# Kernel tuning notes

Hardware: AMD Instinct MI355X
Metric: run time of the kernel (lower is better)

## Reference

```python
import jax, jax.numpy as jnp
import numpy as np

NUM_NODES = 100000
EMBED_DIM = 64
NUM_LAYERS = 3
NUM_EDGES = 3200000


def setup_inputs() -> dict:
    key = jax.random.key(0)
    k_emb, k_edge = jax.random.split(key)
    # Learned node embedding table (PyG LightGCN initializes with xavier-like; values don't matter for correctness)
    emb = jax.random.normal(k_emb, (NUM_NODES, EMBED_DIM), dtype=jnp.float32) * 0.1
    edge_index = jax.random.randint(k_edge, (2, NUM_EDGES), 0, NUM_NODES, dtype=jnp.int64)
    return {"emb": emb, "edge_index": edge_index}


def _lightgcn_embedding(emb, edge_index):
    """Faithful to PyG LightGCN.get_embedding with LGConv (gcn_norm, add_self_loops=False)."""
    n = emb.shape[0]
    src, dst = edge_index[0], edge_index[1]
    # symmetric normalization: deg computed by scatter of ones onto col (dst)
    deg = jax.ops.segment_sum(jnp.ones(src.shape[0], dtype=emb.dtype), dst, num_segments=n)
    deg_inv_sqrt = jnp.where(deg > 0, jax.lax.rsqrt(jnp.maximum(deg, 1.0)), 0.0)
    w = deg_inv_sqrt[src] * deg_inv_sqrt[dst]  # [E]

    x = emb
    out = emb  # alpha-weighted sum; uniform alpha = 1/(num_layers+1)
    for _ in range(NUM_LAYERS):
        # SpMM: out[dst] += w * x[src]
        x = jax.ops.segment_sum(w[:, None] * x[src], dst, num_segments=n)
        out = out + x
    return out / (NUM_LAYERS + 1)


def reference(emb, edge_index):
    return _lightgcn_embedding(emb, edge_index)
```

## Files before the change

### kernel.cpp

```cpp
#include <hip/hip_runtime.h>
#include <hip/hip_bf16.h>

typedef __hip_bfloat16 bf16;
typedef float          f32x4 __attribute__((ext_vector_type(4)));
typedef unsigned short u16x4 __attribute__((ext_vector_type(4)));

#define N_NODES  100000
#define EMBED    64
#define N_EDGES  3200000
#define ND       6400000
#define N_LAYERS 3

#define PNB  256
#define BSZ  391
#define EPB  4096
#define NSL  8
#define SLW  12512
#define R8   (BSZ * NSL)

#define NSPL 4


__global__ void k_flags0(int* f, int* bcnt) {
    int t = threadIdx.x;
    if (t < 16) f[t] = 0;
    bcnt[t] = 0;
}

__global__ void __launch_bounds__(256) k_scan(const uint4* __restrict__ edge4,
                                              const uint4* __restrict__ emb4,
                                              int* __restrict__ fl) {
    __shared__ int red[256];
    __shared__ int rodd[256];
    int t = threadIdx.x;
    int gid = blockIdx.x * 256 + t;
    int step = gridDim.x * 256;

    unsigned odd = 0;
    const int NV_E = (2 * N_EDGES) / 4;
    int i = gid;
    for (; i + 3 * step < NV_E; i += 4 * step) {
        uint4 v0 = edge4[i];
        uint4 v1 = edge4[i + step];
        uint4 v2 = edge4[i + 2 * step];
        uint4 v3 = edge4[i + 3 * step];
        odd |= v0.y | v0.w | v1.y | v1.w | v2.y | v2.w | v3.y | v3.w;
    }
    for (; i < NV_E; i += step) {
        uint4 v = edge4[i];
        odd |= v.y | v.w;
    }

    int local = 0;
    const int NV_M = ND / 8;
#define CEN8(v)                                                          \
    {                                                                    \
        unsigned b;                                                      \
        b = ((v).x >> 8)  & 0x7f; if (b < 0x2e || b > 0x41) local++;     \
        b = ((v).x >> 24) & 0x7f; if (b < 0x2e || b > 0x41) local++;     \
        b = ((v).y >> 8)  & 0x7f; if (b < 0x2e || b > 0x41) local++;     \
        b = ((v).y >> 24) & 0x7f; if (b < 0x2e || b > 0x41) local++;     \
        b = ((v).z >> 8)  & 0x7f; if (b < 0x2e || b > 0x41) local++;     \
        b = ((v).z >> 24) & 0x7f; if (b < 0x2e || b > 0x41) local++;     \
        b = ((v).w >> 8)  & 0x7f; if (b < 0x2e || b > 0x41) local++;     \
        b = ((v).w >> 24) & 0x7f; if (b < 0x2e || b > 0x41) local++;     \
    }
    i = gid;
    for (; i + 3 * step < NV_M; i += 4 * step) {
        uint4 v0 = emb4[i];
        uint4 v1 = emb4[i + step];
        uint4 v2 = emb4[i + 2 * step];
        uint4 v3 = emb4[i + 3 * step];
        CEN8(v0); CEN8(v1); CEN8(v2); CEN8(v3);
    }
    for (; i < NV_M; i += step) {
        uint4 v = emb4[i];
        CEN8(v);
    }
#undef CEN8

    red[t] = local;
    rodd[t] = (odd != 0);
    __syncthreads();
    for (int s2 = 128; s2 > 0; s2 >>= 1) {
        if (t < s2) { red[t] += red[t + s2]; rodd[t] |= rodd[t + s2]; }
        __syncthreads();
    }
    if (t == 0) {
        if (red[0]) atomicAdd(&fl[1], red[0]);
        if (rodd[0]) atomicOr(&fl[0], 1);
    }
}

__device__ __forceinline__ int is_i64(const int* fl) { return fl[0] == 0; }
__device__ __forceinline__ int rd_src(const int* e, int i64, int k) {
    return i64 ? e[2 * k] : e[k];
}
__device__ __forceinline__ int rd_dst(const int* e, int i64, int k) {
    return i64 ? e[2 * (N_EDGES + k)] : e[N_EDGES + k];
}
__device__ __forceinline__ int clampid(int v) {
    return (v < 0) ? 0 : ((v >= N_NODES) ? (N_NODES - 1) : v);
}
__device__ __forceinline__ float rd_emb(const void* emb, const int* fl, int i) {
    if (fl[1] < (ND / 16)) return __bfloat162float(((const bf16*)emb)[i]);
    return ((const float*)emb)[i];
}

__global__ void __launch_bounds__(256) k_bcnt(const int* __restrict__ edge,
                                              const int* __restrict__ fl,
                                              int* __restrict__ bcnt) {
    __shared__ int h[PNB];
    int t = threadIdx.x;
    h[t] = 0;
    __syncthreads();
    const uint4* e4 = (const uint4*)edge;
    int gid = blockIdx.x * 256 + t;
    int step = gridDim.x * 256;
    if (is_i64(fl)) {
        const int base = N_EDGES / 2;
        const int nv   = N_EDGES / 2;
        for (int i = gid; i < nv; i += step) {
            uint4 v = e4[base + i];
            atomicAdd(&h[clampid((int)v.x) / BSZ], 1);
            atomicAdd(&h[clampid((int)v.z) / BSZ], 1);
        }
    } else {
        const int base = N_EDGES / 4;
        const int nv   = N_EDGES / 4;
        for (int i = gid; i < nv; i += step) {
            uint4 v = e4[base + i];
            atomicAdd(&h[clampid((int)v.x) / BSZ], 1);
            atomicAdd(&h[clampid((int)v.y) / BSZ], 1);
            atomicAdd(&h[clampid((int)v.z) / BSZ], 1);
            atomicAdd(&h[clampid((int)v.w) / BSZ], 1);
        }
    }
    __syncthreads();
    if (h[t]) atomicAdd(&bcnt[t], h[t]);
}

__global__ void __launch_bounds__(256) k_bscan(const int* __restrict__ bcnt,
                                               int* __restrict__ bbase,
                                               int* __restrict__ bcur) {
    __shared__ int sb[PNB];
    int t = threadIdx.x;
    int c = bcnt[t];
    sb[t] = c;
    __syncthreads();
    for (int off = 1; off < PNB; off <<= 1) {
        int v = (t >= off) ? sb[t - off] : 0;
        __syncthreads();
        sb[t] += v;
        __syncthreads();
    }
    int ex = sb[t] - c;
    bbase[t] = ex;
    bcur[t] = ex;
    if (t == PNB - 1) bbase[PNB] = sb[t];
}

__global__ void __launch_bounds__(256) k_part(const int* __restrict__ edge,
                                              const int* __restrict__ fl,
                                              int* __restrict__ bcur,
                                              uint2* __restrict__ pairs) {
    __shared__ int h[PNB];
    __shared__ int excl[PNB];
    __shared__ int gbase[PNB];
    __shared__ int lcur[PNB];
    __shared__ uint2 st[EPB];
    __shared__ unsigned char binof[EPB];
    int t = threadIdx.x;
    int e0 = blockIdx.x * EPB;
    int nval = N_EDGES - e0;
    if (nval > EPB) nval = EPB;
    int i64 = is_i64(fl);

    h[t] = 0;
    __syncthreads();
    for (int k = t; k < nval; k += 256) {
        int d = clampid(rd_dst(edge, i64, e0 + k));
        atomicAdd(&h[d / BSZ], 1);
    }
    __syncthreads();
    int c = h[t];
    excl[t] = c;
    __syncthreads();
    for (int off = 1; off < 256; off <<= 1) {
        int v = (t >= off) ? excl[t - off] : 0;
        __syncthreads();
        excl[t] += v;
        __syncthreads();
    }
    int myexcl = excl[t] - c;
    __syncthreads();
    excl[t] = myexcl;
    gbase[t] = (c > 0) ? atomicAdd(&bcur[t], c) : 0;
    lcur[t] = myexcl;
    __syncthreads();
    for (int k = t; k < nval; k += 256) {
        int s = clampid(rd_src(edge, i64, e0 + k));
        int d = clampid(rd_dst(edge, i64, e0 + k));
        int b = d / BSZ;
        int lp = atomicAdd(&lcur[b], 1);
        st[lp] = make_uint2((unsigned)s, (unsigned)d);
        binof[lp] = (unsigned char)b;
    }
    __syncthreads();
    for (int k = t; k < nval; k += 256) {
        int b = binof[k];
        pairs[gbase[b] + (k - excl[b])] = st[k];
    }
}

__global__ void __launch_bounds__(1024) k_build(const uint2* __restrict__ pairs,
                                                const int* __restrict__ bbase,
                                                int* __restrict__ rp2,
                                                float* __restrict__ dis,
                                                int* __restrict__ csr) {
    __shared__ int hh[R8];
    __shared__ int rt[512];
    int b = blockIdx.x;
    int t = threadIdx.x;
    int base = b * BSZ;
    for (int i = t; i < R8; i += 1024) hh[i] = 0;
    __syncthreads();
    int beg = bbase[b], end = bbase[b + 1];
    for (int i = beg + t; i < end; i += 1024) {
        uint2 p = pairs[i];
        int r = (int)p.y - base;
        int s = (int)p.x / SLW;
        atomicAdd(&hh[r * NSL + s], 1);
    }
    __syncthreads();
    int rtot = 0;
    if (t < BSZ) {
        int o = 0;
        for (int k = 0; k < NSL; k++) {
            int cc = hh[t * NSL + k];
            hh[t * NSL + k] = o;
            o += cc;
        }
        rtot = o;
    }
    if (t < 512) rt[t] = (t < BSZ) ? rtot : 0;
    __syncthreads();
    for (int off = 1; off < 512; off <<= 1) {
        int v = 0;
        if (t < 512 && t >= off) v = rt[t - off];
        __syncthreads();
        if (t < 512 && t >= off) rt[t] += v;
        __syncthreads();
    }
    if (t < BSZ) {
        int gb = beg + (rt[t] - rtot);
        int n = base + t;
        if (n < N_NODES) {
            dis[n] = (rtot > 0) ? rsqrtf((float)rtot) : 0.0f;
            for (int k = 0; k < NSL; k++) rp2[n * NSL + k] = gb + hh[t * NSL + k];
            if (n == N_NODES - 1) rp2[N_NODES * NSL] = N_EDGES;
        }
        for (int k = 0; k < NSL; k++) hh[t * NSL + k] += gb;
    }
    __syncthreads();
    for (int i = beg + t; i < end; i += 1024) {
        uint2 p = pairs[i];
        int r = (int)p.y - base;
        int s = (int)p.x / SLW;
        int pos = atomicAdd(&hh[r * NSL + s], 1);
        csr[pos] = (int)p.x;
    }
}

__global__ void k_init(const void* __restrict__ emb, const int* __restrict__ fl,
                       const float* __restrict__ dis,
                       float* __restrict__ out, bf16* __restrict__ Y) {
    int i = blockIdx.x * blockDim.x + threadIdx.x;
    if (i < ND) {
        float v = rd_emb(emb, fl, i);
        out[i] = v;
        int n = i >> 6, cc = i & 63;
        Y[(size_t)(cc >> 4) * (N_NODES * 16) + n * 16 + (cc & 15)] =
            __float2bfloat16(dis[n] * v);
    }
}

#define GATHER4(SRC)                                                     \
    {                                                                    \
        uint2 v = *(const uint2*)(Ys + (SRC) * 8 + c * 2);               \
        a0 += __uint_as_float(v.x << 16);                                \
        a1 += __uint_as_float(v.x & 0xffff0000u);                        \
        a2 += __uint_as_float(v.y << 16);                                \
        a3 += __uint_as_float(v.y & 0xffff0000u);                        \
    }

__global__ void __launch_bounds__(256) k_spmm(
        const int* __restrict__ rp2, const int* __restrict__ csr,
        const float* __restrict__ dis, const bf16* __restrict__ Yin,
        float* __restrict__ out, bf16* __restrict__ Yout, int last) {
    int bid = blockIdx.x;
    int xcd = bid & 7;
    int s = xcd >> 1;
    int rowblk = (bid >> 3) * 2 + (xcd & 1);
    int wave = threadIdx.x >> 6;
    int lane = threadIdx.x & 63;
    int g = lane >> 4;
    int l = lane & 15;
    int e = l >> 2;
    int c = l & 3;
    int n = rowblk * 16 + wave * 4 + g;
    if (n >= N_NODES) return;
    int beg = rp2[n * NSL];
    int end = rp2[(n + 1) * NSL];
    const unsigned* Ys = (const unsigned*)Yin + (size_t)s * (N_NODES * 8);
    float a0 = 0.f, a1 = 0.f, a2 = 0.f, a3 = 0.f;
    int j = beg;
    for (; j + 16 <= end; j += 16) {
        int s0 = csr[j + e];
        int s1 = csr[j + 4 + e];
        int s2 = csr[j + 8 + e];
        int s3 = csr[j + 12 + e];
        GATHER4(s0);
        GATHER4(s1);
        GATHER4(s2);
        GATHER4(s3);
    }
    for (; j + 8 <= end; j += 8) {
        int s0 = csr[j + e];
        int s1 = csr[j + 4 + e];
        GATHER4(s0);
        GATHER4(s1);
    }
    if (j + e < end)     { int sv = csr[j + e];     GATHER4(sv); }
    if (j + 4 + e < end) { int sv = csr[j + 4 + e]; GATHER4(sv); }
    a0 += __shfl_xor(a0, 4); a0 += __shfl_xor(a0, 8);
    a1 += __shfl_xor(a1, 4); a1 += __shfl_xor(a1, 8);
    a2 += __shfl_xor(a2, 4); a2 += __shfl_xor(a2, 8);
    a3 += __shfl_xor(a3, 4); a3 += __shfl_xor(a3, 8);
    if (e == 0) {
        float dn = dis[n];
        float x0 = dn * a0, x1 = dn * a1, x2 = dn * a2, x3 = dn * a3;
        int i4 = n * 16 + s * 4 + c;
        f32x4 o = __builtin_nontemporal_load((const f32x4*)out + i4);
        if (last) {
            o.x = (o.x + x0) * 0.25f;
            o.y = (o.y + x1) * 0.25f;
            o.z = (o.z + x2) * 0.25f;
            o.w = (o.w + x3) * 0.25f;
            __builtin_nontemporal_store(o, (f32x4*)out + i4);
        } else {
            o.x += x0; o.y += x1; o.z += x2; o.w += x3;
            __builtin_nontemporal_store(o, (f32x4*)out + i4);
            bf16 t0 = __float2bfloat16(dn * x0);
            bf16 t1 = __float2bfloat16(dn * x1);
            bf16 t2 = __float2bfloat16(dn * x2);
            bf16 t3 = __float2bfloat16(dn * x3);
            u16x4 yv;
            yv.x = *(unsigned short*)&t0;
            yv.y = *(unsigned short*)&t1;
            yv.z = *(unsigned short*)&t2;
            yv.w = *(unsigned short*)&t3;
            __builtin_nontemporal_store(
                yv, (u16x4*)Yout + (size_t)s * (N_NODES * 4) + n * 4 + c);
        }
    }
}

__global__ void k_fill42(float* __restrict__ o) {
    int i = blockIdx.x * blockDim.x + threadIdx.x;
    if (i < ND) o[i] = 42.0f;
}

extern "C" void kernel_launch(void* const* d_in, const int* in_sizes, int n_in,
                              void* d_out, int out_size, void* d_ws, size_t ws_size,
                              hipStream_t stream) {
    const void* emb = d_in[0];
    const int* edge = (const int*)d_in[1];
    float* out = (float*)d_out;

    const int B = 256;
    const int gND = (ND + B - 1) / B;
    const int gP  = (N_EDGES + EPB - 1) / EPB;
    const int gS  = 25000;

    char* ws = (char*)d_ws;
    int* fl = (int*)ws;
    size_t off = 256;
    const size_t off_dis   = off;  off += (size_t)N_NODES * 4;
    const size_t off_rp2   = off;  off += (size_t)(N_NODES * NSL + 8) * 4;
    const size_t off_bcnt  = off;  off += 1024;
    const size_t off_bbase = off;  off += 1056;
    const size_t off_bcur  = off;  off += 1024;
    const size_t off_csr   = off;  off += (size_t)N_EDGES * 4;
    const size_t off_Y0    = off;  off += (size_t)ND * 2;
    const size_t off_Y1    = off;  off += (size_t)ND * 2;
    const size_t need = off;

    if (ws_size < need) {
        k_fill42<<<gND, B, 0, stream>>>(out);
        return;
    }

    float* dis   = (float*)(ws + off_dis);
    int*   rp2   = (int*)(ws + off_rp2);
    int*   bcnt  = (int*)(ws + off_bcnt);
    int*   bbase = (int*)(ws + off_bbase);
    int*   bcur  = (int*)(ws + off_bcur);
    int*   csr   = (int*)(ws + off_csr);
    uint2* pairs = (uint2*)(ws + off_Y0);
    bf16*  Y0    = (bf16*)(ws + off_Y0);
    bf16*  Y1    = (bf16*)(ws + off_Y1);

    k_flags0<<<1, 256, 0, stream>>>(fl, bcnt);
    k_scan<<<512, B, 0, stream>>>((const uint4*)edge, (const uint4*)emb, fl);

    k_bcnt<<<1024, B, 0, stream>>>(edge, fl, bcnt);
    k_bscan<<<1, 256, 0, stream>>>(bcnt, bbase, bcur);
    k_part<<<gP, B, 0, stream>>>(edge, fl, bcur, pairs);
    k_build<<<PNB, 1024, 0, stream>>>(pairs, bbase, rp2, dis, csr);

    k_init<<<gND, B, 0, stream>>>(emb, fl, dis, out, Y0);

    k_spmm<<<gS, B, 0, stream>>>(rp2, csr, dis, Y0, out, Y1, 0);
    k_spmm<<<gS, B, 0, stream>>>(rp2, csr, dis, Y1, out, Y0, 0);
    k_spmm<<<gS, B, 0, stream>>>(rp2, csr, dis, Y0, out, Y1, 1);
}
```

Baseline: 504.3 us.

## Detect index width from input size, fuse scan with bin count, widen gathers

The edge-index width is now inferred on the host from the input byte size, which removes the full pass over the edge array that checked for nonzero high words. The dtype check on the embeddings is fused with the destination-bin histogram into a single kernel. The partition kernel reads int64 edges as 16-byte vectors. k_init now writes 8 elements per thread, and the SpMM gathers 16-byte bf16 rows with 8 edges per node group instead of 4. The trade-offs are a dependence on in_sizes for choosing the dtype, more registers per SpMM thread and an extra shuffle stage.

```diff
diff --git a/kernel.cpp b/kernel.cpp
--- a/kernel.cpp
+++ b/kernel.cpp
@@ -27,29 +27,27 @@
     bcnt[t] = 0;
 }
 
-__global__ void __launch_bounds__(256) k_scan(const uint4* __restrict__ edge4,
-                                              const uint4* __restrict__ emb4,
-                                              int* __restrict__ fl) {
+__device__ __forceinline__ int rd_src(const int* e, int i64, int k) {
+    return i64 ? e[2 * k] : e[k];
+}
+__device__ __forceinline__ int rd_dst(const int* e, int i64, int k) {
+    return i64 ? e[2 * (N_EDGES + k)] : e[N_EDGES + k];
+}
+__device__ __forceinline__ int clampid(int v) {
+    return (v < 0) ? 0 : ((v >= N_NODES) ? (N_NODES - 1) : v);
+}
+
+__global__ void __launch_bounds__(256) k_scanb(const int* __restrict__ edge,
+                                               const uint4* __restrict__ emb4,
+                                               int i64, int* __restrict__ fl,
+                                               int* __restrict__ bcnt) {
+    __shared__ int h[PNB];
     __shared__ int red[256];
-    __shared__ int rodd[256];
     int t = threadIdx.x;
     int gid = blockIdx.x * 256 + t;
     int step = gridDim.x * 256;
-
-    unsigned odd = 0;
-    const int NV_E = (2 * N_EDGES) / 4;
-    int i = gid;
-    for (; i + 3 * step < NV_E; i += 4 * step) {
-        uint4 v0 = edge4[i];
-        uint4 v1 = edge4[i + step];
-        uint4 v2 = edge4[i + 2 * step];
-        uint4 v3 = edge4[i + 3 * step];
-        odd |= v0.y | v0.w | v1.y | v1.w | v2.y | v2.w | v3.y | v3.w;
-    }
-    for (; i < NV_E; i += step) {
-        uint4 v = edge4[i];
-        odd |= v.y | v.w;
-    }
+    h[t] = 0;
+    __syncthreads();
 
     int local = 0;
     const int NV_M = ND / 8;
@@ -65,7 +63,7 @@
         b = ((v).w >> 8)  & 0x7f; if (b < 0x2e || b > 0x41) local++;     \
         b = ((v).w >> 24) & 0x7f; if (b < 0x2e || b > 0x41) local++;     \
     }
-    i = gid;
+    int i = gid;
     for (; i + 3 * step < NV_M; i += 4 * step) {
         uint4 v0 = emb4[i];
         uint4 v1 = emb4[i + step];
@@ -79,64 +77,34 @@
     }
 #undef CEN8
 
-    red[t] = local;
-    rodd[t] = (odd != 0);
-    __syncthreads();
-    for (int s2 = 128; s2 > 0; s2 >>= 1) {
-        if (t < s2) { red[t] += red[t + s2]; rodd[t] |= rodd[t + s2]; }
-        __syncthreads();
-    }
-    if (t == 0) {
-        if (red[0]) atomicAdd(&fl[1], red[0]);
-        if (rodd[0]) atomicOr(&fl[0], 1);
-    }
-}
-
-__device__ __forceinline__ int is_i64(const int* fl) { return fl[0] == 0; }
-__device__ __forceinline__ int rd_src(const int* e, int i64, int k) {
-    return i64 ? e[2 * k] : e[k];
-}
-__device__ __forceinline__ int rd_dst(const int* e, int i64, int k) {
-    return i64 ? e[2 * (N_EDGES + k)] : e[N_EDGES + k];
-}
-__device__ __forceinline__ int clampid(int v) {
-    return (v < 0) ? 0 : ((v >= N_NODES) ? (N_NODES - 1) : v);
-}
-__device__ __forceinline__ float rd_emb(const void* emb, const int* fl, int i) {
-    if (fl[1] < (ND / 16)) return __bfloat162float(((const bf16*)emb)[i]);
-    return ((const float*)emb)[i];
-}
-
-__global__ void __launch_bounds__(256) k_bcnt(const int* __restrict__ edge,
-                                              const int* __restrict__ fl,
-                                              int* __restrict__ bcnt) {
-    __shared__ int h[PNB];
-    int t = threadIdx.x;
-    h[t] = 0;
-    __syncthreads();
     const uint4* e4 = (const uint4*)edge;
-    int gid = blockIdx.x * 256 + t;
-    int step = gridDim.x * 256;
-    if (is_i64(fl)) {
+    if (i64) {
         const int base = N_EDGES / 2;
         const int nv   = N_EDGES / 2;
-        for (int i = gid; i < nv; i += step) {
-            uint4 v = e4[base + i];
+        for (int k = gid; k < nv; k += step) {
+            uint4 v = e4[base + k];
             atomicAdd(&h[clampid((int)v.x) / BSZ], 1);
             atomicAdd(&h[clampid((int)v.z) / BSZ], 1);
         }
     } else {
         const int base = N_EDGES / 4;
         const int nv   = N_EDGES / 4;
-        for (int i = gid; i < nv; i += step) {
-            uint4 v = e4[base + i];
+        for (int k = gid; k < nv; k += step) {
+            uint4 v = e4[base + k];
             atomicAdd(&h[clampid((int)v.x) / BSZ], 1);
             atomicAdd(&h[clampid((int)v.y) / BSZ], 1);
             atomicAdd(&h[clampid((int)v.z) / BSZ], 1);
             atomicAdd(&h[clampid((int)v.w) / BSZ], 1);
         }
     }
-    __syncthreads();
+
+    red[t] = local;
+    __syncthreads();
+    for (int s2 = 128; s2 > 0; s2 >>= 1) {
+        if (t < s2) red[t] += red[t + s2];
+        __syncthreads();
+    }
+    if (t == 0 && red[0]) atomicAdd(&fl[1], red[0]);
     if (h[t]) atomicAdd(&bcnt[t], h[t]);
 }
 
@@ -161,7 +129,7 @@
 }
 
 __global__ void __launch_bounds__(256) k_part(const int* __restrict__ edge,
-                                              const int* __restrict__ fl,
+                                              int i64,
                                               int* __restrict__ bcur,
                                               uint2* __restrict__ pairs) {
     __shared__ int h[PNB];
@@ -174,13 +142,22 @@
     int e0 = blockIdx.x * EPB;
     int nval = N_EDGES - e0;
     if (nval > EPB) nval = EPB;
-    int i64 = is_i64(fl);
+    const uint4* e4 = (const uint4*)edge;
 
     h[t] = 0;
     __syncthreads();
-    for (int k = t; k < nval; k += 256) {
-        int d = clampid(rd_dst(edge, i64, e0 + k));
-        atomicAdd(&h[d / BSZ], 1);
+    if (i64) {
+        int half = nval >> 1;
+        for (int m = t; m < half; m += 256) {
+            uint4 v = e4[(size_t)(N_EDGES / 2) + (e0 >> 1) + m];
+            atomicAdd(&h[clampid((int)v.x) / BSZ], 1);
+            atomicAdd(&h[clampid((int)v.z) / BSZ], 1);
+        }
+    } else {
+        for (int k = t; k < nval; k += 256) {
+            int d = clampid(rd_dst(edge, 0, e0 + k));
+            atomicAdd(&h[d / BSZ], 1);
+        }
     }
     __syncthreads();
     int c = h[t];
@@ -198,13 +175,31 @@
     gbase[t] = (c > 0) ? atomicAdd(&bcur[t], c) : 0;
     lcur[t] = myexcl;
     __syncthreads();
-    for (int k = t; k < nval; k += 256) {
-        int s = clampid(rd_src(edge, i64, e0 + k));
-        int d = clampid(rd_dst(edge, i64, e0 + k));
-        int b = d / BSZ;
-        int lp = atomicAdd(&lcur[b], 1);
-        st[lp] = make_uint2((unsigned)s, (unsigned)d);
-        binof[lp] = (unsigned char)b;
+    if (i64) {
+        int half = nval >> 1;
+        for (int m = t; m < half; m += 256) {
+            uint4 vs = e4[(e0 >> 1) + m];
+            uint4 vd = e4[(size_t)(N_EDGES / 2) + (e0 >> 1) + m];
+            int s0 = clampid((int)vs.x), d0 = clampid((int)vd.x);
+            int b0 = d0 / BSZ;
+            int lp0 = atomicAdd(&lcur[b0], 1);
+            st[lp0] = make_uint2((unsigned)s0, (unsigned)d0);
+            binof[lp0] = (unsigned char)b0;
+            int s1 = clampid((int)vs.z), d1 = clampid((int)vd.z);
+            int b1 = d1 / BSZ;
+            int lp1 = atomicAdd(&lcur[b1], 1);
+            st[lp1] = make_uint2((unsigned)s1, (unsigned)d1);
+            binof[lp1] = (unsigned char)b1;
+        }
+    } else {
+        for (int k = t; k < nval; k += 256) {
+            int s = clampid(rd_src(edge, 0, e0 + k));
+            int d = clampid(rd_dst(edge, 0, e0 + k));
+            int b = d / BSZ;
+            int lp = atomicAdd(&lcur[b], 1);
+            st[lp] = make_uint2((unsigned)s, (unsigned)d);
+            binof[lp] = (unsigned char)b;
+        }
     }
     __syncthreads();
     for (int k = t; k < nval; k += 256) {
@@ -272,26 +267,57 @@
     }
 }
 
-__global__ void k_init(const void* __restrict__ emb, const int* __restrict__ fl,
-                       const float* __restrict__ dis,
-                       float* __restrict__ out, bf16* __restrict__ Y) {
-    int i = blockIdx.x * blockDim.x + threadIdx.x;
-    if (i < ND) {
-        float v = rd_emb(emb, fl, i);
-        out[i] = v;
-        int n = i >> 6, cc = i & 63;
-        Y[(size_t)(cc >> 4) * (N_NODES * 16) + n * 16 + (cc & 15)] =
-            __float2bfloat16(dis[n] * v);
-    }
-}
-
-#define GATHER4(SRC)                                                     \
+__global__ void __launch_bounds__(256) k_init(const void* __restrict__ emb,
+                                              const int* __restrict__ fl,
+                                              const float* __restrict__ dis,
+                                              float* __restrict__ out,
+                                              bf16* __restrict__ Y) {
+    int idx = blockIdx.x * 256 + threadIdx.x;
+    if (idx >= ND / 8) return;
+    int n = idx >> 3;
+    int g = idx & 7;
+    float dn = dis[n];
+    float f[8];
+    if (fl[1] < (ND / 16)) {
+        const bf16* eb = (const bf16*)emb + (size_t)idx * 8;
+        for (int k = 0; k < 8; k++) f[k] = __bfloat162float(eb[k]);
+    } else {
+        const f32x4* e4 = (const f32x4*)emb + (size_t)idx * 2;
+        f32x4 a = e4[0], b = e4[1];
+        f[0] = a.x; f[1] = a.y; f[2] = a.z; f[3] = a.w;
+        f[4] = b.x; f[5] = b.y; f[6] = b.z; f[7] = b.w;
+    }
+    f32x4* o4 = (f32x4*)out + (size_t)idx * 2;
+    f32x4 oa, ob;
+    oa.x = f[0]; oa.y = f[1]; oa.z = f[2]; oa.w = f[3];
+    ob.x = f[4]; ob.y = f[5]; ob.z = f[6]; ob.w = f[7];
+    o4[0] = oa; o4[1] = ob;
+    int s = g >> 1;
+    u16x4* yp = (u16x4*)Y + (size_t)s * (N_NODES * 4) + n * 4 + (g & 1) * 2;
+    u16x4 y0, y1;
+    bf16 tb;
+    tb = __float2bfloat16(dn * f[0]); y0.x = *(unsigned short*)&tb;
+    tb = __float2bfloat16(dn * f[1]); y0.y = *(unsigned short*)&tb;
+    tb = __float2bfloat16(dn * f[2]); y0.z = *(unsigned short*)&tb;
+    tb = __float2bfloat16(dn * f[3]); y0.w = *(unsigned short*)&tb;
+    tb = __float2bfloat16(dn * f[4]); y1.x = *(unsigned short*)&tb;
+    tb = __float2bfloat16(dn * f[5]); y1.y = *(unsigned short*)&tb;
+    tb = __float2bfloat16(dn * f[6]); y1.z = *(unsigned short*)&tb;
+    tb = __float2bfloat16(dn * f[7]); y1.w = *(unsigned short*)&tb;
+    yp[0] = y0; yp[1] = y1;
+}
+
+#define GATHER8(SRC)                                                     \
     {                                                                    \
-        uint2 v = *(const uint2*)(Ys + (SRC) * 8 + c * 2);               \
+        uint4 v = Ys[(size_t)(SRC) * 2 + c];                             \
         a0 += __uint_as_float(v.x << 16);                                \
         a1 += __uint_as_float(v.x & 0xffff0000u);                        \
         a2 += __uint_as_float(v.y << 16);                                \
         a3 += __uint_as_float(v.y & 0xffff0000u);                        \
+        a4 += __uint_as_float(v.z << 16);                                \
+        a5 += __uint_as_float(v.z & 0xffff0000u);                        \
+        a6 += __uint_as_float(v.w << 16);                                \
+        a7 += __uint_as_float(v.w & 0xffff0000u);                        \
     }
 
 __global__ void __launch_bounds__(256) k_spmm(
@@ -304,64 +330,83 @@
     int rowblk = (bid >> 3) * 2 + (xcd & 1);
     int wave = threadIdx.x >> 6;
     int lane = threadIdx.x & 63;
-    int g = lane >> 4;
     int l = lane & 15;
-    int e = l >> 2;
-    int c = l & 3;
-    int n = rowblk * 16 + wave * 4 + g;
+    int e = l >> 1;
+    int c = l & 1;
+    int n = rowblk * 16 + wave * 4 + (lane >> 4);
     if (n >= N_NODES) return;
     int beg = rp2[n * NSL];
     int end = rp2[(n + 1) * NSL];
-    const unsigned* Ys = (const unsigned*)Yin + (size_t)s * (N_NODES * 8);
+    const uint4* Ys = (const uint4*)Yin + (size_t)s * (N_NODES * 2);
     float a0 = 0.f, a1 = 0.f, a2 = 0.f, a3 = 0.f;
+    float a4 = 0.f, a5 = 0.f, a6 = 0.f, a7 = 0.f;
     int j = beg;
-    for (; j + 16 <= end; j += 16) {
+    for (; j + 32 <= end; j += 32) {
         int s0 = csr[j + e];
-        int s1 = csr[j + 4 + e];
-        int s2 = csr[j + 8 + e];
-        int s3 = csr[j + 12 + e];
-        GATHER4(s0);
-        GATHER4(s1);
-        GATHER4(s2);
-        GATHER4(s3);
-    }
-    for (; j + 8 <= end; j += 8) {
+        int s1 = csr[j + 8 + e];
+        int s2 = csr[j + 16 + e];
+        int s3 = csr[j + 24 + e];
+        GATHER8(s0);
+        GATHER8(s1);
+        GATHER8(s2);
+        GATHER8(s3);
+    }
+    if (j + 16 <= end) {
         int s0 = csr[j + e];
-        int s1 = csr[j + 4 + e];
-        GATHER4(s0);
-        GATHER4(s1);
-    }
-    if (j + e < end)     { int sv = csr[j + e];     GATHER4(sv); }
-    if (j + 4 + e < end) { int sv = csr[j + 4 + e]; GATHER4(sv); }
-    a0 += __shfl_xor(a0, 4); a0 += __shfl_xor(a0, 8);
-    a1 += __shfl_xor(a1, 4); a1 += __shfl_xor(a1, 8);
-    a2 += __shfl_xor(a2, 4); a2 += __shfl_xor(a2, 8);
-    a3 += __shfl_xor(a3, 4); a3 += __shfl_xor(a3, 8);
+        int s1 = csr[j + 8 + e];
+        GATHER8(s0);
+        GATHER8(s1);
+        j += 16;
+    }
+    if (j + 8 <= end) {
+        int s0 = csr[j + e];
+        GATHER8(s0);
+        j += 8;
+    }
+    if (j + e < end) {
+        int sv = csr[j + e];
+        GATHER8(sv);
+    }
+    a0 += __shfl_xor(a0, 2); a0 += __shfl_xor(a0, 4); a0 += __shfl_xor(a0, 8);
+    a1 += __shfl_xor(a1, 2); a1 += __shfl_xor(a1, 4); a1 += __shfl_xor(a1, 8);
+    a2 += __shfl_xor(a2, 2); a2 += __shfl_xor(a2, 4); a2 += __shfl_xor(a2, 8);
+    a3 += __shfl_xor(a3, 2); a3 += __shfl_xor(a3, 4); a3 += __shfl_xor(a3, 8);
+    a4 += __shfl_xor(a4, 2); a4 += __shfl_xor(a4, 4); a4 += __shfl_xor(a4, 8);
+    a5 += __shfl_xor(a5, 2); a5 += __shfl_xor(a5, 4); a5 += __shfl_xor(a5, 8);
+    a6 += __shfl_xor(a6, 2); a6 += __shfl_xor(a6, 4); a6 += __shfl_xor(a6, 8);
+    a7 += __shfl_xor(a7, 2); a7 += __shfl_xor(a7, 4); a7 += __shfl_xor(a7, 8);
     if (e == 0) {
         float dn = dis[n];
+        int i8 = n * 16 + s * 4 + c * 2;
+        f32x4 oa = __builtin_nontemporal_load((const f32x4*)out + i8);
+        f32x4 ob = __builtin_nontemporal_load((const f32x4*)out + i8 + 1);
         float x0 = dn * a0, x1 = dn * a1, x2 = dn * a2, x3 = dn * a3;
-        int i4 = n * 16 + s * 4 + c;
-        f32x4 o = __builtin_nontemporal_load((const f32x4*)out + i4);
+        float x4 = dn * a4, x5 = dn * a5, x6 = dn * a6, x7 = dn * a7;
         if (last) {
-            o.x = (o.x + x0) * 0.25f;
-            o.y = (o.y + x1) * 0.25f;
-            o.z = (o.z + x2) * 0.25f;
-            o.w = (o.w + x3) * 0.25f;
-            __builtin_nontemporal_store(o, (f32x4*)out + i4);
+            oa.x = (oa.x + x0) * 0.25f; oa.y = (oa.y + x1) * 0.25f;
+            oa.z = (oa.z + x2) * 0.25f; oa.w = (oa.w + x3) * 0.25f;
+            ob.x = (ob.x + x4) * 0.25f; ob.y = (ob.y + x5) * 0.25f;
+            ob.z = (ob.z + x6) * 0.25f; ob.w = (ob.w + x7) * 0.25f;
+            __builtin_nontemporal_store(oa, (f32x4*)out + i8);
+            __builtin_nontemporal_store(ob, (f32x4*)out + i8 + 1);
         } else {
-            o.x += x0; o.y += x1; o.z += x2; o.w += x3;
-            __builtin_nontemporal_store(o, (f32x4*)out + i4);
-            bf16 t0 = __float2bfloat16(dn * x0);
-            bf16 t1 = __float2bfloat16(dn * x1);
-            bf16 t2 = __float2bfloat16(dn * x2);
-            bf16 t3 = __float2bfloat16(dn * x3);
-            u16x4 yv;
-            yv.x = *(unsigned short*)&t0;
-            yv.y = *(unsigned short*)&t1;
-            yv.z = *(unsigned short*)&t2;
-            yv.w = *(unsigned short*)&t3;
-            __builtin_nontemporal_store(
-                yv, (u16x4*)Yout + (size_t)s * (N_NODES * 4) + n * 4 + c);
+            oa.x += x0; oa.y += x1; oa.z += x2; oa.w += x3;
+            ob.x += x4; ob.y += x5; ob.z += x6; ob.w += x7;
+            __builtin_nontemporal_store(oa, (f32x4*)out + i8);
+            __builtin_nontemporal_store(ob, (f32x4*)out + i8 + 1);
+            u16x4 y0, y1;
+            bf16 tb;
+            tb = __float2bfloat16(dn * x0); y0.x = *(unsigned short*)&tb;
+            tb = __float2bfloat16(dn * x1); y0.y = *(unsigned short*)&tb;
+            tb = __float2bfloat16(dn * x2); y0.z = *(unsigned short*)&tb;
+            tb = __float2bfloat16(dn * x3); y0.w = *(unsigned short*)&tb;
+            tb = __float2bfloat16(dn * x4); y1.x = *(unsigned short*)&tb;
+            tb = __float2bfloat16(dn * x5); y1.y = *(unsigned short*)&tb;
+            tb = __float2bfloat16(dn * x6); y1.z = *(unsigned short*)&tb;
+            tb = __float2bfloat16(dn * x7); y1.w = *(unsigned short*)&tb;
+            u16x4* yp = (u16x4*)Yout + (size_t)s * (N_NODES * 4) + n * 4 + c * 2;
+            __builtin_nontemporal_store(y0, yp);
+            __builtin_nontemporal_store(y1, yp + 1);
         }
     }
 }
@@ -378,8 +423,12 @@
     const int* edge = (const int*)d_in[1];
     float* out = (float*)d_out;
 
+    const long long i64_bytes = 2LL * N_EDGES * 8;
+    int i64 = (in_sizes[1] >= (int)i64_bytes) ? 1 : 0;
+
     const int B = 256;
     const int gND = (ND + B - 1) / B;
+    const int gI  = (ND / 8 + B - 1) / B;
     const int gP  = (N_EDGES + EPB - 1) / EPB;
     const int gS  = 25000;
 
@@ -412,14 +461,13 @@
     bf16*  Y1    = (bf16*)(ws + off_Y1);
 
     k_flags0<<<1, 256, 0, stream>>>(fl, bcnt);
-    k_scan<<<512, B, 0, stream>>>((const uint4*)edge, (const uint4*)emb, fl);
-
-    k_bcnt<<<1024, B, 0, stream>>>(edge, fl, bcnt);
+    k_scanb<<<512, B, 0, stream>>>(edge, (const uint4*)emb, i64, fl, bcnt);
+
     k_bscan<<<1, 256, 0, stream>>>(bcnt, bbase, bcur);
-    k_part<<<gP, B, 0, stream>>>(edge, fl, bcur, pairs);
+    k_part<<<gP, B, 0, stream>>>(edge, i64, bcur, pairs);
     k_build<<<PNB, 1024, 0, stream>>>(pairs, bbase, rp2, dis, csr);
 
-    k_init<<<gND, B, 0, stream>>>(emb, fl, dis, out, Y0);
+    k_init<<<gI, B, 0, stream>>>(emb, fl, dis, out, Y0);
 
     k_spmm<<<gS, B, 0, stream>>>(rp2, csr, dis, Y0, out, Y1, 0);
     k_spmm<<<gS, B, 0, stream>>>(rp2, csr, dis, Y1, out, Y0, 0);
```

Measured after the change: 473.4 us. 6.1% less time.
